# Kernel tuning notes

Measured on AMD Instinct MI355X. Metric: run time of the kernel, lower is better.

Reference implementation:

```python
import jax, jax.numpy as jnp
import numpy as np

QUERY_DIM = 256
CONTEXT_DIM = 256
N_HEADS = 4
D_HEAD = QUERY_DIM // N_HEADS
LN_EPS = 1e-5


def setup_inputs() -> dict:
    key = jax.random.key(0)
    ks = jax.random.split(key, 8)
    B, L, Nv = 4, 8192, 8
    query = jax.random.normal(ks[0], (B, L, QUERY_DIM), dtype=jnp.float32)
    context = jax.random.normal(ks[1], (B, L, Nv, CONTEXT_DIM), dtype=jnp.float32)
    s = 1.0 / np.sqrt(CONTEXT_DIM)
    Wk = jax.random.uniform(ks[2], (CONTEXT_DIM, QUERY_DIM), jnp.float32, -s, s)
    bk = jax.random.uniform(ks[3], (QUERY_DIM,), jnp.float32, -s, s)
    Wv = jax.random.uniform(ks[4], (CONTEXT_DIM, QUERY_DIM), jnp.float32, -s, s)
    bv = jax.random.uniform(ks[5], (QUERY_DIM,), jnp.float32, -s, s)
    gamma = jnp.ones((QUERY_DIM,), jnp.float32)
    beta = jnp.zeros((QUERY_DIM,), jnp.float32)
    return {"query": query, "context": context, "Wk": Wk, "bk": bk,
            "Wv": Wv, "bv": bv, "gamma": gamma, "beta": beta}


def reference(query, context, Wk, bk, Wv, bv, gamma, beta):
    B, L, C = query.shape
    Nv = context.shape[2]
    # LayerNorm over channel dim
    mu = jnp.mean(query, axis=-1, keepdims=True)
    var = jnp.mean(jnp.square(query - mu), axis=-1, keepdims=True)
    q = (query - mu) * jax.lax.rsqrt(var + LN_EPS) * gamma + beta
    # projections: [B,L,Nv,C]
    k = context @ Wk + bk
    v = context @ Wv + bv
    q = q.reshape(B, L, N_HEADS, D_HEAD)
    k = k.reshape(B, L, Nv, N_HEADS, D_HEAD)
    v = v.reshape(B, L, Nv, N_HEADS, D_HEAD)
    # per-token attention over the Nv local context elements
    scores = jnp.einsum('blhd,blnhd->bhln', q, k) / np.sqrt(D_HEAD)
    probs = jax.nn.softmax(scores, axis=-1)  # [B,H,L,Nv]
    out = jnp.einsum('bhln,blnhd->blhd', probs, v).reshape(B, L, C)
    return out, probs
```

## Files before the change

kernel.cpp:

```cpp
#include <hip/hip_runtime.h>
#include <math.h>

#define TB     16
#define CDIM   256
#define NHEADS 4
#define DHEAD  64
#define NV     8
#define LSEQ   8192
#define NB     4

typedef short  bf16x8 __attribute__((ext_vector_type(8)));
typedef float  f32x4  __attribute__((ext_vector_type(4)));
typedef unsigned short u16;

static __device__ __forceinline__ u16 f2bf(float x) {
    unsigned u = __float_as_uint(x);
    unsigned r = ((u >> 16) & 1u) + 0x7fffu;
    return (u16)((u + r) >> 16);
}
static __device__ __forceinline__ float bf2f(u16 h) {
    return __uint_as_float(((unsigned)h) << 16);
}

__global__ __launch_bounds__(256) void prep_frags(
    const float* __restrict__ Wk, const float* __restrict__ Wv,
    u16* __restrict__ wkf, u16* __restrict__ wvf)
{
    const int tid = blockIdx.x * 256 + threadIdx.x;
    union { u16 u[8]; uint4 v; } pk;
    if (tid < 16384) {
        int l = tid & 63; int r = tid >> 6;
        const int s  = r & 1;  r >>= 1;
        const int nt = r & 15; r >>= 4;
        const int kc = r & 1;  r >>= 1;
        const int h  = r & 3;
        const int c     = nt * 16 + (l & 15);
        const int dbase = h * DHEAD + kc * 32 + (l >> 4) * 8;
        #pragma unroll
        for (int j = 0; j < 8; ++j) {
            const float x  = Wk[(size_t)c * CDIM + dbase + j] * 0.125f;
            const u16 hi = f2bf(x);
            const u16 lo = f2bf(x - bf2f(hi));
            pk.u[j] = s ? lo : hi;
        }
        *reinterpret_cast<uint4*>(wkf + (size_t)tid * 8) = pk.v;
    } else if (tid < 32768) {
        int t2 = tid - 16384;
        int l = t2 & 63; int r = t2 >> 6;
        const int s  = r & 1; r >>= 1;
        const int nt = r & 3; r >>= 2;
        const int kc = r & 7; r >>= 3;
        const int h  = r & 3;
        const int d     = h * DHEAD + nt * 16 + (l & 15);
        const int cbase = kc * 32 + (l >> 4) * 8;
        #pragma unroll
        for (int j = 0; j < 8; ++j) {
            const float x  = Wv[(size_t)(cbase + j) * CDIM + d];
            const u16 hi = f2bf(x);
            const u16 lo = f2bf(x - bf2f(hi));
            pk.u[j] = s ? lo : hi;
        }
        *reinterpret_cast<uint4*>(wvf + (size_t)t2 * 8) = pk.v;
    }
}

__global__ __launch_bounds__(1024, 8) void triplane_fused(
    const float* __restrict__ q,
    const float* __restrict__ ctx,
    const u16*   __restrict__ wkf,
    const u16*   __restrict__ wvf,
    const float* __restrict__ bv,
    const float* __restrict__ gamma,
    const float* __restrict__ beta,
    float* __restrict__ out,
    float* __restrict__ probs_out)
{
    __shared__ __align__(16) float s_qk[TB * NHEADS * CDIM];
    __shared__ __align__(16) u16   s_qnh[TB * CDIM];
    __shared__ __align__(16) u16   s_qnl[TB * CDIM];

    const int tid  = threadIdx.x;
    const int w    = tid >> 6;
    const int lane = tid & 63;
    const int tok0 = blockIdx.x * TB;
    const f32x4 zero4 = {0.f, 0.f, 0.f, 0.f};

    const int h  = w & 3;
    const int cq = w >> 2;

    {
        const int t = w;
        const int c = lane * 4;
        const float4 qv = *reinterpret_cast<const float4*>(q + (size_t)(tok0 + t) * CDIM + c);
        float s  = qv.x + qv.y + qv.z + qv.w;
        float s2 = qv.x*qv.x + qv.y*qv.y + qv.z*qv.z + qv.w*qv.w;
        #pragma unroll
        for (int off = 32; off >= 1; off >>= 1) {
            s  += __shfl_xor(s,  off);
            s2 += __shfl_xor(s2, off);
        }
        const float mu   = s  * (1.0f / CDIM);
        const float var  = s2 * (1.0f / CDIM) - mu * mu;
        const float rstd = rsqrtf(var + 1e-5f);
        const float4 g  = *reinterpret_cast<const float4*>(gamma + c);
        const float4 be = *reinterpret_cast<const float4*>(beta + c);
        float qn[4];
        qn[0] = (qv.x - mu) * rstd * g.x + be.x;
        qn[1] = (qv.y - mu) * rstd * g.y + be.y;
        qn[2] = (qv.z - mu) * rstd * g.z + be.z;
        qn[3] = (qv.w - mu) * rstd * g.w + be.w;
        ushort4 vh, vl;
        u16 h0 = f2bf(qn[0]); vh.x = h0; vl.x = f2bf(qn[0] - bf2f(h0));
        u16 h1 = f2bf(qn[1]); vh.y = h1; vl.y = f2bf(qn[1] - bf2f(h1));
        u16 h2 = f2bf(qn[2]); vh.z = h2; vl.z = f2bf(qn[2] - bf2f(h2));
        u16 h3 = f2bf(qn[3]); vh.w = h3; vl.w = f2bf(qn[3] - bf2f(h3));
        const int off = t * 512 + ((lane * 8) ^ (t << 4));
        *reinterpret_cast<ushort4*>(reinterpret_cast<char*>(s_qnh) + off) = vh;
        *reinterpret_cast<ushort4*>(reinterpret_cast<char*>(s_qnl) + off) = vl;
    }
    __syncthreads();

    {
        const int arow = lane & 15;
        const int akq  = lane >> 4;
        bf16x8 aH[2], aL[2];
        #pragma unroll
        for (int kc = 0; kc < 2; ++kc) {
            const int intra = (h * DHEAD + kc * 32 + akq * 8) * 2;
            const int off   = arow * 512 + (intra ^ (arow << 4));
            aH[kc] = *reinterpret_cast<const bf16x8*>(reinterpret_cast<const char*>(s_qnh) + off);
            aL[kc] = *reinterpret_cast<const bf16x8*>(reinterpret_cast<const char*>(s_qnl) + off);
        }
        #pragma unroll
        for (int nt = 0; nt < 4; ++nt) {
            const int ntg = cq * 4 + nt;
            f32x4 acc = zero4;
            #pragma unroll
            for (int kc = 0; kc < 2; ++kc) {
                const u16* p = wkf + ((size_t)(h * 4096 + kc * 2048 + ntg * 128) + lane) * 8;
                const bf16x8 bH = *reinterpret_cast<const bf16x8*>(p);
                acc = __builtin_amdgcn_mfma_f32_16x16x32_bf16(aH[kc], bH, acc, 0, 0, 0);
                acc = __builtin_amdgcn_mfma_f32_16x16x32_bf16(aL[kc], bH, acc, 0, 0, 0);
            }
            const int cc = ntg * 16 + (lane & 15);
            #pragma unroll
            for (int reg = 0; reg < 4; ++reg) {
                const int t = (lane >> 4) * 4 + reg;
                s_qk[(t * NHEADS + h) * CDIM + cc] = acc[reg];
            }
        }
    }
    __syncthreads();

    float p0, p1, p2, p3;
    {
        const int t  = w;
        const int cs = lane & 7;
        const float* cb = ctx + ((size_t)(tok0 + t) * NV + (lane >> 3)) * CDIM + cs * 4;
        p0 = 0.f; p1 = 0.f; p2 = 0.f; p3 = 0.f;
        #pragma unroll
        for (int i = 0; i < 8; ++i) {
            const int c = i * 32 + cs * 4;
            const float4 cv = *reinterpret_cast<const float4*>(cb + i * 32);
            const float4 k0 = *reinterpret_cast<const float4*>(&s_qk[(t*NHEADS+0)*CDIM + c]);
            const float4 k1 = *reinterpret_cast<const float4*>(&s_qk[(t*NHEADS+1)*CDIM + c]);
            const float4 k2 = *reinterpret_cast<const float4*>(&s_qk[(t*NHEADS+2)*CDIM + c]);
            const float4 k3 = *reinterpret_cast<const float4*>(&s_qk[(t*NHEADS+3)*CDIM + c]);
            p0 += cv.x*k0.x + cv.y*k0.y + cv.z*k0.z + cv.w*k0.w;
            p1 += cv.x*k1.x + cv.y*k1.y + cv.z*k1.z + cv.w*k1.w;
            p2 += cv.x*k2.x + cv.y*k2.y + cv.z*k2.z + cv.w*k2.w;
            p3 += cv.x*k3.x + cv.y*k3.y + cv.z*k3.z + cv.w*k3.w;
        }
        #pragma unroll
        for (int off = 4; off >= 1; off >>= 1) {
            p0 += __shfl_xor(p0, off);
            p1 += __shfl_xor(p1, off);
            p2 += __shfl_xor(p2, off);
            p3 += __shfl_xor(p3, off);
        }
        float m0 = p0, m1 = p1, m2 = p2, m3 = p3;
        #pragma unroll
        for (int off = 8; off <= 32; off <<= 1) {
            m0 = fmaxf(m0, __shfl_xor(m0, off));
            m1 = fmaxf(m1, __shfl_xor(m1, off));
            m2 = fmaxf(m2, __shfl_xor(m2, off));
            m3 = fmaxf(m3, __shfl_xor(m3, off));
        }
        p0 = __expf(p0 - m0); p1 = __expf(p1 - m1);
        p2 = __expf(p2 - m2); p3 = __expf(p3 - m3);
        float s0 = p0, s1 = p1, s2 = p2, s3 = p3;
        #pragma unroll
        for (int off = 8; off <= 32; off <<= 1) {
            s0 += __shfl_xor(s0, off);
            s1 += __shfl_xor(s1, off);
            s2 += __shfl_xor(s2, off);
            s3 += __shfl_xor(s3, off);
        }
        p0 /= s0; p1 /= s1; p2 /= s2; p3 /= s3;
        if (cs == 0) {
            const int tok = tok0 + t;
            const int b = tok >> 13;
            const int l = tok & (LSEQ - 1);
            const int n = lane >> 3;
            float* pb = probs_out + (((size_t)b * NHEADS) * LSEQ + l) * NV + n;
            pb[0 * LSEQ * NV] = p0;
            pb[1 * LSEQ * NV] = p1;
            pb[2 * LSEQ * NV] = p2;
            pb[3 * LSEQ * NV] = p3;
        }
    }
    __syncthreads();

    {
        const int t = w;
        const float* cbase = ctx + ((size_t)(tok0 + t) * NV) * CDIM + lane * 4;
        float4 a0, a1, a2, a3;
        a0.x=a0.y=a0.z=a0.w=0.f; a1=a0; a2=a0; a3=a0;
        #pragma unroll
        for (int n = 0; n < NV; ++n) {
            const float prx = __shfl(p0, n * 8);
            const float pry = __shfl(p1, n * 8);
            const float prz = __shfl(p2, n * 8);
            const float prw = __shfl(p3, n * 8);
            const float4 cv = *reinterpret_cast<const float4*>(cbase + (size_t)n * CDIM);
            a0.x += prx*cv.x; a0.y += prx*cv.y; a0.z += prx*cv.z; a0.w += prx*cv.w;
            a1.x += pry*cv.x; a1.y += pry*cv.y; a1.z += pry*cv.z; a1.w += pry*cv.w;
            a2.x += prz*cv.x; a2.y += prz*cv.y; a2.z += prz*cv.z; a2.w += prz*cv.w;
            a3.x += prw*cv.x; a3.y += prw*cv.y; a3.z += prw*cv.z; a3.w += prw*cv.w;
        }
        char* wch = reinterpret_cast<char*>(s_qk);
        const int xo = (lane * 8) ^ (t << 4);
        #pragma unroll
        for (int hh = 0; hh < 4; ++hh) {
            const float4 v = (hh == 0) ? a0 : (hh == 1) ? a1 : (hh == 2) ? a2 : a3;
            ushort4 vh;
            vh.x = f2bf(v.x); vh.y = f2bf(v.y); vh.z = f2bf(v.z); vh.w = f2bf(v.w);
            const int off = (hh * TB + t) * 512 + xo;
            *reinterpret_cast<ushort4*>(wch + off) = vh;
        }
    }
    __syncthreads();

    {
        const int arow = lane & 15;
        const int akq  = lane >> 4;
        const int nt   = cq;
        const char* wch = reinterpret_cast<const char*>(s_qk);
        const u16* wvbase = wvf + ((size_t)(h * 4096) + lane) * 8;
        f32x4 acc = zero4;
        #pragma unroll
        for (int kc = 0; kc < 8; ++kc) {
            const int intra = (kc * 32 + akq * 8) * 2;
            const int off   = (h * TB + arow) * 512 + (intra ^ (arow << 4));
            const bf16x8 aH = *reinterpret_cast<const bf16x8*>(wch + off);
            const u16* pp = wvbase + (size_t)(kc * 512 + nt * 128) * 8;
            const bf16x8 bH = *reinterpret_cast<const bf16x8*>(pp);
            acc = __builtin_amdgcn_mfma_f32_16x16x32_bf16(aH, bH, acc, 0, 0, 0);
        }
        const int d = h * DHEAD + nt * 16 + (lane & 15);
        const float bvv = bv[d];
        #pragma unroll
        for (int reg = 0; reg < 4; ++reg) {
            const int t = (lane >> 4) * 4 + reg;
            out[(size_t)(tok0 + t) * CDIM + d] = acc[reg] + bvv;
        }
    }
}

#define TBF 8
__global__ __launch_bounds__(512, 6) void triplane_fused_v1(
    const float* __restrict__ q, const float* __restrict__ ctx,
    const float* __restrict__ Wk, const float* __restrict__ Wv,
    const float* __restrict__ bv, const float* __restrict__ gamma,
    const float* __restrict__ beta, float* __restrict__ out,
    float* __restrict__ probs_out)
{
    __shared__ float s_qn[TBF * CDIM];
    __shared__ float s_qk[TBF * NHEADS * CDIM];
    __shared__ float s_sc[TBF * NV * NHEADS];
    const int tid  = threadIdx.x;
    const int w    = tid >> 6;
    const int lane = tid & 63;
    const int tok0 = blockIdx.x * TBF;
    {
        const int t = w; const int c = lane * 4;
        const float4 qv = *reinterpret_cast<const float4*>(q + (size_t)(tok0 + t) * CDIM + c);
        float s  = qv.x + qv.y + qv.z + qv.w;
        float s2 = qv.x*qv.x + qv.y*qv.y + qv.z*qv.z + qv.w*qv.w;
        #pragma unroll
        for (int off = 32; off >= 1; off >>= 1) { s += __shfl_xor(s, off); s2 += __shfl_xor(s2, off); }
        const float mu = s * (1.0f/CDIM);
        const float var = s2 * (1.0f/CDIM) - mu*mu;
        const float rstd = rsqrtf(var + 1e-5f);
        const float4 g  = *reinterpret_cast<const float4*>(gamma + c);
        const float4 be = *reinterpret_cast<const float4*>(beta + c);
        float4 qn;
        qn.x=(qv.x-mu)*rstd*g.x+be.x; qn.y=(qv.y-mu)*rstd*g.y+be.y;
        qn.z=(qv.z-mu)*rstd*g.z+be.z; qn.w=(qv.w-mu)*rstd*g.w+be.w;
        *reinterpret_cast<float4*>(&s_qn[t*CDIM + c]) = qn;
    }
    __syncthreads();
    {
        const int h = w & 3; const int cg = w >> 2;
        const int c0 = cg*128 + lane; const int c1 = c0 + 64;
        const float* wk0 = Wk + (size_t)c0*CDIM + h*DHEAD;
        const float* wk1 = Wk + (size_t)c1*CDIM + h*DHEAD;
        float acc0[TBF], acc1[TBF];
        #pragma unroll
        for (int t = 0; t < TBF; ++t) { acc0[t]=0.f; acc1[t]=0.f; }
        for (int d4 = 0; d4 < DHEAD/4; ++d4) {
            const float4 wa = *reinterpret_cast<const float4*>(wk0 + d4*4);
            const float4 wb = *reinterpret_cast<const float4*>(wk1 + d4*4);
            #pragma unroll
            for (int t = 0; t < TBF; ++t) {
                const float4 qv = *reinterpret_cast<const float4*>(&s_qn[t*CDIM + h*DHEAD + d4*4]);
                acc0[t] += qv.x*wa.x + qv.y*wa.y + qv.z*wa.z + qv.w*wa.w;
                acc1[t] += qv.x*wb.x + qv.y*wb.y + qv.z*wb.z + qv.w*wb.w;
            }
        }
        #pragma unroll
        for (int t = 0; t < TBF; ++t) {
            s_qk[(t*NHEADS+h)*CDIM + c0] = acc0[t];
            s_qk[(t*NHEADS+h)*CDIM + c1] = acc1[t];
        }
    }
    __syncthreads();
    {
        const int t = w; const int n = lane >> 3; const int cs = lane & 7;
        const float* cb = ctx + ((size_t)(tok0 + t)*NV + n)*CDIM;
        float p0=0,p1=0,p2=0,p3=0;
        #pragma unroll
        for (int i = 0; i < 8; ++i) {
            const int c = i*32 + cs*4;
            const float4 cv = *reinterpret_cast<const float4*>(cb + c);
            const float4 k0 = *reinterpret_cast<const float4*>(&s_qk[(t*NHEADS+0)*CDIM + c]);
            const float4 k1 = *reinterpret_cast<const float4*>(&s_qk[(t*NHEADS+1)*CDIM + c]);
            const float4 k2 = *reinterpret_cast<const float4*>(&s_qk[(t*NHEADS+2)*CDIM + c]);
            const float4 k3 = *reinterpret_cast<const float4*>(&s_qk[(t*NHEADS+3)*CDIM + c]);
            p0 += cv.x*k0.x+cv.y*k0.y+cv.z*k0.z+cv.w*k0.w;
            p1 += cv.x*k1.x+cv.y*k1.y+cv.z*k1.z+cv.w*k1.w;
            p2 += cv.x*k2.x+cv.y*k2.y+cv.z*k2.z+cv.w*k2.w;
            p3 += cv.x*k3.x+cv.y*k3.y+cv.z*k3.z+cv.w*k3.w;
        }
        #pragma unroll
        for (int off = 4; off >= 1; off >>= 1) {
            p0 += __shfl_xor(p0, off); p1 += __shfl_xor(p1, off);
            p2 += __shfl_xor(p2, off); p3 += __shfl_xor(p3, off);
        }
        if (cs == 0) {
            s_sc[(t*NV+n)*NHEADS+0] = p0*0.125f; s_sc[(t*NV+n)*NHEADS+1] = p1*0.125f;
            s_sc[(t*NV+n)*NHEADS+2] = p2*0.125f; s_sc[(t*NV+n)*NHEADS+3] = p3*0.125f;
        }
    }
    __syncthreads();
    float* s_out = s_qn;
    {
        float4 z; z.x=z.y=z.z=z.w=0.f;
        reinterpret_cast<float4*>(s_out)[tid] = z;
        if (tid < TBF*NHEADS) {
            const int t = tid >> 2; const int h = tid & 3;
            float sc[NV]; float m = -1e30f;
            #pragma unroll
            for (int n = 0; n < NV; ++n) { sc[n] = s_sc[(t*NV+n)*NHEADS+h]; m = fmaxf(m, sc[n]); }
            float sum = 0.f;
            #pragma unroll
            for (int n = 0; n < NV; ++n) { sc[n] = __expf(sc[n]-m); sum += sc[n]; }
            const float inv = 1.f/sum;
            const int tok = tok0 + t; const int b = tok >> 13; const int l = tok & (LSEQ-1);
            float* pdst = probs_out + (((size_t)b*NHEADS + h)*LSEQ + l)*NV;
            #pragma unroll
            for (int n = 0; n < NV; ++n) { const float p = sc[n]*inv; s_sc[(t*NV+n)*NHEADS+h] = p; pdst[n] = p; }
        }
    }
    __syncthreads();
    {
        const int t = w;
        const float* cbase = ctx + ((size_t)(tok0 + t)*NV)*CDIM;
        float4 a0,a1,a2,a3; a0.x=a0.y=a0.z=a0.w=0.f; a1=a0; a2=a0; a3=a0;
        for (int n = 0; n < NV; ++n) {
            const float4 pr = *reinterpret_cast<const float4*>(&s_sc[(t*NV+n)*NHEADS]);
            const float4 cv = *reinterpret_cast<const float4*>(cbase + (size_t)n*CDIM + lane*4);
            a0.x+=pr.x*cv.x; a0.y+=pr.x*cv.y; a0.z+=pr.x*cv.z; a0.w+=pr.x*cv.w;
            a1.x+=pr.y*cv.x; a1.y+=pr.y*cv.y; a1.z+=pr.y*cv.z; a1.w+=pr.y*cv.w;
            a2.x+=pr.z*cv.x; a2.y+=pr.z*cv.y; a2.z+=pr.z*cv.z; a2.w+=pr.z*cv.w;
            a3.x+=pr.w*cv.x; a3.y+=pr.w*cv.y; a3.z+=pr.w*cv.z; a3.w+=pr.w*cv.w;
        }
        *reinterpret_cast<float4*>(&s_qk[(t*NHEADS+0)*CDIM + lane*4]) = a0;
        *reinterpret_cast<float4*>(&s_qk[(t*NHEADS+1)*CDIM + lane*4]) = a1;
        *reinterpret_cast<float4*>(&s_qk[(t*NHEADS+2)*CDIM + lane*4]) = a2;
        *reinterpret_cast<float4*>(&s_qk[(t*NHEADS+3)*CDIM + lane*4]) = a3;
    }
    __syncthreads();
    {
        const int h = w & 3; const int cg = w >> 2;
        float acc[TBF];
        #pragma unroll
        for (int t = 0; t < TBF; ++t) acc[t] = 0.f;
        const float* wvbase = Wv + h*DHEAD + lane;
        for (int c4 = 0; c4 < 32; ++c4) {
            const int c = cg*128 + c4*4;
            const float wv0 = wvbase[(size_t)(c+0)*CDIM];
            const float wv1 = wvbase[(size_t)(c+1)*CDIM];
            const float wv2 = wvbase[(size_t)(c+2)*CDIM];
            const float wv3 = wvbase[(size_t)(c+3)*CDIM];
            #pragma unroll
            for (int t = 0; t < TBF; ++t) {
                const float4 wc = *reinterpret_cast<const float4*>(&s_qk[(t*NHEADS+h)*CDIM + c]);
                acc[t] += wc.x*wv0 + wc.y*wv1 + wc.z*wv2 + wc.w*wv3;
            }
        }
        #pragma unroll
        for (int t = 0; t < TBF; ++t) atomicAdd(&s_out[t*CDIM + h*DHEAD + lane], acc[t]);
    }
    __syncthreads();
    {
        const int t = w; const int c = lane * 4;
        float4 o = *reinterpret_cast<const float4*>(&s_out[t*CDIM + c]);
        const float4 bvv = *reinterpret_cast<const float4*>(bv + c);
        o.x += bvv.x; o.y += bvv.y; o.z += bvv.z; o.w += bvv.w;
        *reinterpret_cast<float4*>(out + (size_t)(tok0 + t)*CDIM + c) = o;
    }
}

extern "C" void kernel_launch(void* const* d_in, const int* in_sizes, int n_in,
                              void* d_out, int out_size, void* d_ws, size_t ws_size,
                              hipStream_t stream) {
    const float* q     = (const float*)d_in[0];
    const float* ctx   = (const float*)d_in[1];
    const float* Wk    = (const float*)d_in[2];
    const float* Wv    = (const float*)d_in[4];
    const float* bv    = (const float*)d_in[5];
    const float* gamma = (const float*)d_in[6];
    const float* beta  = (const float*)d_in[7];

    float* out   = (float*)d_out;
    float* probs = out + (size_t)NB * LSEQ * CDIM;

    const int n_tok = NB * LSEQ;
    const size_t ws_need = (size_t)2 * 131072 * sizeof(u16);

    if (d_ws != nullptr && ws_size >= ws_need) {
        u16* wkf = (u16*)d_ws;
        u16* wvf = wkf + 131072;
        hipLaunchKernelGGL(prep_frags, dim3(128), dim3(256), 0, stream, Wk, Wv, wkf, wvf);
        hipLaunchKernelGGL(triplane_fused, dim3(n_tok / TB), dim3(1024), 0, stream,
                           q, ctx, wkf, wvf, bv, gamma, beta, out, probs);
    } else {
        hipLaunchKernelGGL(triplane_fused_v1, dim3(n_tok / TBF), dim3(512), 0, stream,
                           q, ctx, Wk, Wv, bv, gamma, beta, out, probs);
    }
}
```

Measured before the change: 106.0 us.

## Drop bf16 low-part split for query and remove a barrier via per-token layout

Removes the hi/lo bf16 split of the normalized query, which halves the MFMA count in the q·Wk projection and drops one shared-memory buffer. The weighted-context staging area is re-laid out so each token's rows occupy their own 4KB slice of s_qk, with the swizzle adjusted to match. This lets the __syncthreads between the softmax stage and the context-write stage be removed. The cost is reduced precision in the query-key scores, and the barrier removal depends on no wave still reading s_qk rows that another wave overwrites.

```diff
diff --git a/kernel.cpp b/kernel.cpp
--- a/kernel.cpp
+++ b/kernel.cpp
@@ -77,7 +77,6 @@
 {
     __shared__ __align__(16) float s_qk[TB * NHEADS * CDIM];
     __shared__ __align__(16) u16   s_qnh[TB * CDIM];
-    __shared__ __align__(16) u16   s_qnl[TB * CDIM];
 
     const int tid  = threadIdx.x;
     const int w    = tid >> 6;
@@ -104,32 +103,25 @@
         const float rstd = rsqrtf(var + 1e-5f);
         const float4 g  = *reinterpret_cast<const float4*>(gamma + c);
         const float4 be = *reinterpret_cast<const float4*>(beta + c);
-        float qn[4];
-        qn[0] = (qv.x - mu) * rstd * g.x + be.x;
-        qn[1] = (qv.y - mu) * rstd * g.y + be.y;
-        qn[2] = (qv.z - mu) * rstd * g.z + be.z;
-        qn[3] = (qv.w - mu) * rstd * g.w + be.w;
-        ushort4 vh, vl;
-        u16 h0 = f2bf(qn[0]); vh.x = h0; vl.x = f2bf(qn[0] - bf2f(h0));
-        u16 h1 = f2bf(qn[1]); vh.y = h1; vl.y = f2bf(qn[1] - bf2f(h1));
-        u16 h2 = f2bf(qn[2]); vh.z = h2; vl.z = f2bf(qn[2] - bf2f(h2));
-        u16 h3 = f2bf(qn[3]); vh.w = h3; vl.w = f2bf(qn[3] - bf2f(h3));
+        ushort4 vh;
+        vh.x = f2bf((qv.x - mu) * rstd * g.x + be.x);
+        vh.y = f2bf((qv.y - mu) * rstd * g.y + be.y);
+        vh.z = f2bf((qv.z - mu) * rstd * g.z + be.z);
+        vh.w = f2bf((qv.w - mu) * rstd * g.w + be.w);
         const int off = t * 512 + ((lane * 8) ^ (t << 4));
         *reinterpret_cast<ushort4*>(reinterpret_cast<char*>(s_qnh) + off) = vh;
-        *reinterpret_cast<ushort4*>(reinterpret_cast<char*>(s_qnl) + off) = vl;
     }
     __syncthreads();
 
     {
         const int arow = lane & 15;
         const int akq  = lane >> 4;
-        bf16x8 aH[2], aL[2];
+        bf16x8 aH[2];
         #pragma unroll
         for (int kc = 0; kc < 2; ++kc) {
             const int intra = (h * DHEAD + kc * 32 + akq * 8) * 2;
             const int off   = arow * 512 + (intra ^ (arow << 4));
             aH[kc] = *reinterpret_cast<const bf16x8*>(reinterpret_cast<const char*>(s_qnh) + off);
-            aL[kc] = *reinterpret_cast<const bf16x8*>(reinterpret_cast<const char*>(s_qnl) + off);
         }
         #pragma unroll
         for (int nt = 0; nt < 4; ++nt) {
@@ -140,7 +132,6 @@
                 const u16* p = wkf + ((size_t)(h * 4096 + kc * 2048 + ntg * 128) + lane) * 8;
                 const bf16x8 bH = *reinterpret_cast<const bf16x8*>(p);
                 acc = __builtin_amdgcn_mfma_f32_16x16x32_bf16(aH[kc], bH, acc, 0, 0, 0);
-                acc = __builtin_amdgcn_mfma_f32_16x16x32_bf16(aL[kc], bH, acc, 0, 0, 0);
             }
             const int cc = ntg * 16 + (lane & 15);
             #pragma unroll
@@ -209,7 +200,6 @@
             pb[3 * LSEQ * NV] = p3;
         }
     }
-    __syncthreads();
 
     {
         const int t = w;
@@ -228,15 +218,14 @@
             a2.x += prz*cv.x; a2.y += prz*cv.y; a2.z += prz*cv.z; a2.w += prz*cv.w;
             a3.x += prw*cv.x; a3.y += prw*cv.y; a3.z += prw*cv.z; a3.w += prw*cv.w;
         }
-        char* wch = reinterpret_cast<char*>(s_qk);
-        const int xo = (lane * 8) ^ (t << 4);
+        char* base = reinterpret_cast<char*>(s_qk) + t * 4096;
+        const int xo = (lane * 8) ^ ((t & 7) << 4);
         #pragma unroll
         for (int hh = 0; hh < 4; ++hh) {
             const float4 v = (hh == 0) ? a0 : (hh == 1) ? a1 : (hh == 2) ? a2 : a3;
             ushort4 vh;
             vh.x = f2bf(v.x); vh.y = f2bf(v.y); vh.z = f2bf(v.z); vh.w = f2bf(v.w);
-            const int off = (hh * TB + t) * 512 + xo;
-            *reinterpret_cast<ushort4*>(wch + off) = vh;
+            *reinterpret_cast<ushort4*>(base + hh * 512 + xo) = vh;
         }
     }
     __syncthreads();
@@ -250,8 +239,8 @@
         f32x4 acc = zero4;
         #pragma unroll
         for (int kc = 0; kc < 8; ++kc) {
-            const int intra = (kc * 32 + akq * 8) * 2;
-            const int off   = (h * TB + arow) * 512 + (intra ^ (arow << 4));
+            const int intra = kc * 64 + akq * 16;
+            const int off   = arow * 4096 + h * 512 + (intra ^ ((arow & 7) << 4));
             const bf16x8 aH = *reinterpret_cast<const bf16x8*>(wch + off);
             const u16* pp = wvbase + (size_t)(kc * 512 + nt * 128) * 8;
             const bf16x8 bH = *reinterpret_cast<const bf16x8*>(pp);
```

New measurement: 101.5 us. 4.2% less time.
